# Optimization experiments

Hardware: AMD Instinct MI355X
Metric: run time of the kernel (lower is better)

Reference implementation:

```python
import jax, jax.numpy as jnp
import numpy as np

DIM = 1024
SEQ = 4096


def setup_inputs() -> dict:
    key = jax.random.key(0)
    ks = jax.random.split(key, 7)
    s = 1.0 / np.sqrt(DIM)
    return {
        "X": jax.random.normal(ks[0], (SEQ, DIM), dtype=jnp.float32),
        "Wq": jax.random.uniform(ks[1], (DIM, DIM), jnp.float32, -s, s),
        "bq": jax.random.uniform(ks[2], (DIM,), jnp.float32, -s, s),
        "Wk": jax.random.uniform(ks[3], (DIM, DIM), jnp.float32, -s, s),
        "bk": jax.random.uniform(ks[4], (DIM,), jnp.float32, -s, s),
        "Wv": jax.random.uniform(ks[5], (DIM, DIM), jnp.float32, -s, s),
        "bv": jax.random.uniform(ks[6], (DIM,), jnp.float32, -s, s),
    }


def reference(X, Wq, bq, Wk, bk, Wv, bv):
    # QKV projections (nn.Linear: x @ W.T + b); here W stored as [in, out]
    Q = X @ Wq + bq            # [S, D]
    K = X @ Wk + bk            # [S, D]
    V = X @ Wv + bv            # [S, D]
    scale = 1.0 / jnp.sqrt(jnp.asarray(X.shape[-1], X.dtype))
    scores = (Q @ K.T) * scale  # [S, S]
    attn = jax.nn.softmax(scores, axis=-1)
    return attn @ V            # [S, D]
```

## Files before the change

kernel.cpp:

```cpp
#include <hip/hip_runtime.h>

typedef unsigned short u16;
typedef unsigned int u32;
typedef __bf16 bf16x8 __attribute__((ext_vector_type(8)));
typedef float f32x4 __attribute__((ext_vector_type(4)));
typedef u16 u16x4 __attribute__((ext_vector_type(4)));

__device__ __forceinline__ u16 f32_to_bf16(float f) {
    u32 u = __builtin_bit_cast(u32, f);
    u32 r = (u + 0x7fffu + ((u >> 16) & 1u)) >> 16;
    return (u16)r;
}

__device__ __forceinline__ void async_cp16(const u16* g, u16* l) {
    __builtin_amdgcn_global_load_lds(
        (const __attribute__((address_space(1))) u32*)g,
        (__attribute__((address_space(3))) u32*)l, 16, 0, 0);
}

#define GEMM_PROLOG(Aptr, Bptr, LDA, LDB)                                     \
    __shared__ u16 lds[16384];                                                \
    const int tid  = threadIdx.x;                                             \
    const int wid  = tid >> 6;                                                \
    const int lane = tid & 63;                                                \
    const int s0 = wid * 2, s1 = s0 + 1;                                      \
    const int rr = lane >> 2;                                                 \
    const int cc = (lane & 3) * 8;                                            \
    const u16* gA0 = (Aptr) + (size_t)(bm + s0 * 16 + rr) * (LDA) + cc;       \
    const u16* gA1 = (Aptr) + (size_t)(bm + s1 * 16 + rr) * (LDA) + cc;       \
    const u16* gB0 = (Bptr) + (size_t)(bn + s0 * 16 + rr) * (LDB) + cc;       \
    const u16* gB1 = (Bptr) + (size_t)(bn + s1 * 16 + rr) * (LDB) + cc;       \
    u16* lA0  = &lds[s0 * 512];                                               \
    u16* lA1  = &lds[s1 * 512];                                               \
    u16* lA0h = lA0 + 4096;                                                   \
    u16* lA1h = lA1 + 4096;                                                   \
    u16* lB0  = &lds[8192 + s0 * 512];                                        \
    u16* lB1  = &lds[8192 + s1 * 512];                                        \
    u16* lB0h = lB0 + 4096;                                                   \
    u16* lB1h = lB1 + 4096;                                                   \
    const int wm = (wid >> 1) * 64;                                           \
    const int wn = (wid & 1) * 64;                                            \
    const int row16 = lane & 15;                                              \
    const int quad  = lane >> 4;                                              \
    f32x4 acc[4][4];                                                          \
    const f32x4 zero = {0.f, 0.f, 0.f, 0.f};                                  \
    _Pragma("unroll")                                                         \
    for (int i = 0; i < 4; i++)                                               \
        _Pragma("unroll")                                                     \
        for (int j = 0; j < 4; j++) acc[i][j] = zero;

#define GEMM_KLOOP(KLEN)                                                      \
    for (int kt = 0; kt < (KLEN); kt += 64) {                                 \
        __syncthreads();                                                      \
        async_cp16(gA0, lA0);                                                 \
        async_cp16(gA1, lA1);                                                 \
        async_cp16(gA0 + 32, lA0h);                                           \
        async_cp16(gA1 + 32, lA1h);                                           \
        async_cp16(gB0, lB0);                                                 \
        async_cp16(gB1, lB1);                                                 \
        async_cp16(gB0 + 32, lB0h);                                           \
        async_cp16(gB1 + 32, lB1h);                                           \
        gA0 += 64; gA1 += 64; gB0 += 64; gB1 += 64;                           \
        __syncthreads();                                                      \
        _Pragma("unroll")                                                     \
        for (int h = 0; h < 2; h++) {                                         \
            bf16x8 fa[4], fb[4];                                              \
            _Pragma("unroll")                                                 \
            for (int im = 0; im < 4; im++)                                    \
                fa[im] = *(const bf16x8*)&lds[h * 4096 + (wm + im * 16 + row16) * 32 + quad * 8]; \
            _Pragma("unroll")                                                 \
            for (int in = 0; in < 4; in++)                                    \
                fb[in] = *(const bf16x8*)&lds[8192 + h * 4096 + (wn + in * 16 + row16) * 32 + quad * 8]; \
            _Pragma("unroll")                                                 \
            for (int im = 0; im < 4; im++)                                    \
                _Pragma("unroll")                                             \
                for (int in = 0; in < 4; in++)                                \
                    acc[im][in] = __builtin_amdgcn_mfma_f32_16x16x32_bf16(    \
                        fa[im], fb[in], acc[im][in], 0, 0, 0);                \
        }                                                                     \
    }

#define SWIZZLE_2D()                                                          \
    const int L   = blockIdx.x;                                               \
    const int id2 = L & 255;                                                  \
    const int bm  = (((id2 & 7) * 4) + (id2 >> 6)) * 128;                     \
    const int bn  = (((id2 >> 3) & 7) + (L >> 8) * 8) * 128;

__global__ __launch_bounds__(256, 4)
void gemm_qkv(const u16* __restrict__ A, const u16* __restrict__ B,
              u16* __restrict__ C, u16* __restrict__ Vt,
              const float* __restrict__ bias,
              int K, int lda, int ldb, int ldc)
{
    SWIZZLE_2D()
    GEMM_PROLOG(A, B, lda, ldb)
    GEMM_KLOOP(K)
    if (bn < 2048) {
        #pragma unroll
        for (int im = 0; im < 4; im++) {
            #pragma unroll
            for (int in = 0; in < 4; in++) {
                const int n = bn + wn + in * 16 + row16;
                const float bv = bias[n];
                #pragma unroll
                for (int r = 0; r < 4; r++) {
                    const int m = bm + wm + im * 16 + quad * 4 + r;
                    C[(size_t)m * ldc + n] = f32_to_bf16(acc[im][in][r] + bv);
                }
            }
        }
    } else {
        #pragma unroll
        for (int im = 0; im < 4; im++) {
            #pragma unroll
            for (int in = 0; in < 4; in++) {
                const int n = bn + wn + in * 16 + row16;
                const float bv = bias[n];
                const int d = n - 2048;
                const int m = bm + wm + im * 16 + quad * 4;
                u16x4 pk;
                #pragma unroll
                for (int r = 0; r < 4; r++)
                    pk[r] = f32_to_bf16(acc[im][in][r] + bv);
                *(u16x4*)&Vt[(size_t)d * 4096 + m] = pk;
            }
        }
    }
}

__global__ __launch_bounds__(256, 4)
void gemm_score_exp(const u16* __restrict__ A, const u16* __restrict__ B,
                    u16* __restrict__ P, float* __restrict__ rowsum,
                    int K, int lda, int ldb, int ldc, float scale)
{
    SWIZZLE_2D()
    GEMM_PROLOG(A, B, lda, ldb)
    GEMM_KLOOP(K)
    #pragma unroll
    for (int im = 0; im < 4; im++) {
        #pragma unroll
        for (int r = 0; r < 4; r++) {
            const int m = bm + wm + im * 16 + quad * 4 + r;
            float rs = 0.f;
            #pragma unroll
            for (int in = 0; in < 4; in++) {
                const int n = bn + wn + in * 16 + row16;
                float e = __expf(acc[im][in][r] * scale);
                P[(size_t)m * ldc + n] = f32_to_bf16(e);
                rs += e;
            }
            rs += __shfl_xor(rs, 1);
            rs += __shfl_xor(rs, 2);
            rs += __shfl_xor(rs, 4);
            rs += __shfl_xor(rs, 8);
            if (row16 == 0) atomicAdd(&rowsum[m], rs);
        }
    }
}

__global__ __launch_bounds__(256, 4)
void gemm_pv_splitk(const u16* __restrict__ A, const u16* __restrict__ B,
                    float* __restrict__ C0, float* __restrict__ C1,
                    float* __restrict__ C2, float* __restrict__ C3,
                    int Kq, int lda, int ldb, int ldc)
{
    const int id2 = blockIdx.x;
    const int bm  = (((id2 & 7) * 4) + (id2 >> 6)) * 128;
    const int bn  = ((id2 >> 3) & 7) * 128;
    const int z   = blockIdx.y;
    float* C = (z == 0) ? C0 : (z == 1) ? C1 : (z == 2) ? C2 : C3;
    const int koff = z * Kq;
    GEMM_PROLOG(A + koff, B + koff, lda, ldb)
    GEMM_KLOOP(Kq)
    #pragma unroll
    for (int im = 0; im < 4; im++) {
        #pragma unroll
        for (int in = 0; in < 4; in++) {
            const int n = bn + wn + in * 16 + row16;
            #pragma unroll
            for (int r = 0; r < 4; r++) {
                const int m = bm + wm + im * 16 + quad * 4 + r;
                C[(size_t)m * ldc + n] = acc[im][in][r];
            }
        }
    }
}

__global__ __launch_bounds__(256)
void reduce4_scale(float4* __restrict__ out, const float4* __restrict__ p1,
                   const float4* __restrict__ p2, const float4* __restrict__ p3,
                   const float* __restrict__ rowsum)
{
    const int i = blockIdx.x * 256 + threadIdx.x;
    const float inv = 1.0f / rowsum[i >> 8];
    float4 a = out[i], b = p1[i], c = p2[i], d = p3[i];
    a.x = (a.x + b.x + c.x + d.x) * inv;
    a.y = (a.y + b.y + c.y + d.y) * inv;
    a.z = (a.z + b.z + c.z + d.z) * inv;
    a.w = (a.w + b.w + c.w + d.w) * inv;
    out[i] = a;
}

__global__ __launch_bounds__(256)
void convert_x(const float4* __restrict__ X, uint2* __restrict__ Xb)
{
    const int i = blockIdx.x * 256 + threadIdx.x;
    float4 v = X[i];
    uint2 o;
    o.x = (u32)f32_to_bf16(v.x) | ((u32)f32_to_bf16(v.y) << 16);
    o.y = (u32)f32_to_bf16(v.z) | ((u32)f32_to_bf16(v.w) << 16);
    Xb[i] = o;
}

__global__ __launch_bounds__(256)
void transpose_w3(const float* __restrict__ W0, const float* __restrict__ W1,
                  const float* __restrict__ W2, u16* __restrict__ Wt)
{
    __shared__ float t[32][33];
    const int z  = blockIdx.z;
    const float* W = (z == 0) ? W0 : (z == 1) ? W1 : W2;
    u16* dst = Wt + (size_t)z * 1024 * 1024;
    const int bk = blockIdx.x * 32;
    const int bn = blockIdx.y * 32;
    const int tx = threadIdx.x & 31;
    const int ty = threadIdx.x >> 5;
    #pragma unroll
    for (int i = 0; i < 32; i += 8)
        t[ty + i][tx] = W[(size_t)(bk + ty + i) * 1024 + bn + tx];
    __syncthreads();
    #pragma unroll
    for (int i = 0; i < 32; i += 8)
        dst[(size_t)(bn + ty + i) * 1024 + bk + tx] = f32_to_bf16(t[tx][ty + i]);
}

__global__ __launch_bounds__(256)
void prep(const float* __restrict__ bq, const float* __restrict__ bk,
          const float* __restrict__ bv, float* __restrict__ b3,
          float* __restrict__ rowsum)
{
    const int i = blockIdx.x * 256 + threadIdx.x;
    if (i < 3072)
        b3[i] = (i < 1024) ? bq[i] : (i < 2048) ? bk[i - 1024] : bv[i - 2048];
    else
        rowsum[i - 3072] = 0.f;
}

extern "C" void kernel_launch(void* const* d_in, const int* in_sizes, int n_in,
                              void* d_out, int out_size, void* d_ws, size_t ws_size,
                              hipStream_t stream)
{
    const float* X  = (const float*)d_in[0];
    const float* Wq = (const float*)d_in[1];
    const float* bq = (const float*)d_in[2];
    const float* Wk = (const float*)d_in[3];
    const float* bk = (const float*)d_in[4];
    const float* Wv = (const float*)d_in[5];
    const float* bv = (const float*)d_in[6];
    float* out = (float*)d_out;

    char* ws = (char*)d_ws;
    u16*   P      = (u16*)ws;
    u16*   Xb     = (u16*)ws;
    u16*   WqkvT  = (u16*)(ws + (8u << 20));
    float* rowsum = (float*)(ws + (32u << 20));
    float* bias3  = (float*)(ws + (32u << 20) + (64u << 10));
    u16*   QKV    = (u16*)(ws + (33u << 20));
    float* p1     = (float*)(ws + (33u << 20));
    float* p2     = (float*)(ws + (49u << 20));
    float* p3     = (float*)(ws + (65u << 20));
    u16*   Vt     = (u16*)(ws + (82u << 20));

    convert_x<<<4096, 256, 0, stream>>>((const float4*)X, (uint2*)Xb);
    transpose_w3<<<dim3(32, 32, 3), 256, 0, stream>>>(Wq, Wk, Wv, WqkvT);
    prep<<<28, 256, 0, stream>>>(bq, bk, bv, bias3, rowsum);

    gemm_qkv<<<768, 256, 0, stream>>>(Xb, WqkvT, QKV, Vt, bias3,
        1024, 1024, 1024, 3072);

    gemm_score_exp<<<1024, 256, 0, stream>>>(QKV, QKV + 1024, P, rowsum,
        1024, 3072, 3072, 4096, 0.03125f);

    gemm_pv_splitk<<<dim3(256, 4), 256, 0, stream>>>(P, Vt, out, p1, p2, p3,
        1024, 4096, 4096, 1024);

    reduce4_scale<<<4096, 256, 0, stream>>>((float4*)out, (const float4*)p1,
        (const float4*)p2, (const float4*)p3, rowsum);
}
```

Baseline: 215.3 us.

## Double-buffer GEMM K-loop with async prefetch and merge prep kernels into one launch

The shared GEMM K-loop changes from 64-wide steps with two barriers per step to 32-wide steps over two ping-pong LDS buffers. The next tile's async global-to-LDS copy is issued before computing on the current tile, so load latency overlaps MFMA work and only one barrier per iteration remains. Separately, the three preprocessing kernels (X conversion, weight transpose, bias/rowsum init) are merged into one launch dispatched by block index, saving two kernel launches. The change relies on the async copies of the previous iteration being complete at the barrier, and halving the K step doubles the number of loop iterations.

```diff
diff --git a/kernel.cpp b/kernel.cpp
--- a/kernel.cpp
+++ b/kernel.cpp
@@ -32,12 +32,8 @@
     const u16* gB1 = (Bptr) + (size_t)(bn + s1 * 16 + rr) * (LDB) + cc;       \
     u16* lA0  = &lds[s0 * 512];                                               \
     u16* lA1  = &lds[s1 * 512];                                               \
-    u16* lA0h = lA0 + 4096;                                                   \
-    u16* lA1h = lA1 + 4096;                                                   \
-    u16* lB0  = &lds[8192 + s0 * 512];                                        \
-    u16* lB1  = &lds[8192 + s1 * 512];                                        \
-    u16* lB0h = lB0 + 4096;                                                   \
-    u16* lB1h = lB1 + 4096;                                                   \
+    u16* lB0  = &lds[4096 + s0 * 512];                                        \
+    u16* lB1  = &lds[4096 + s1 * 512];                                        \
     const int wm = (wid >> 1) * 64;                                           \
     const int wn = (wid & 1) * 64;                                            \
     const int row16 = lane & 15;                                              \
@@ -50,27 +46,31 @@
         for (int j = 0; j < 4; j++) acc[i][j] = zero;
 
 #define GEMM_KLOOP(KLEN)                                                      \
-    for (int kt = 0; kt < (KLEN); kt += 64) {                                 \
-        __syncthreads();                                                      \
+    {                                                                         \
         async_cp16(gA0, lA0);                                                 \
         async_cp16(gA1, lA1);                                                 \
-        async_cp16(gA0 + 32, lA0h);                                           \
-        async_cp16(gA1 + 32, lA1h);                                           \
         async_cp16(gB0, lB0);                                                 \
         async_cp16(gB1, lB1);                                                 \
-        async_cp16(gB0 + 32, lB0h);                                           \
-        async_cp16(gB1 + 32, lB1h);                                           \
-        gA0 += 64; gA1 += 64; gB0 += 64; gB1 += 64;                           \
-        __syncthreads();                                                      \
-        _Pragma("unroll")                                                     \
-        for (int h = 0; h < 2; h++) {                                         \
+        gA0 += 32; gA1 += 32; gB0 += 32; gB1 += 32;                           \
+        const int NIT = (KLEN) >> 5;                                          \
+        for (int it = 0; it < NIT; ++it) {                                    \
+            const int cur = (it & 1) << 13;       \
+            const int nxt = 8192 - cur;                                       \
+            __syncthreads();       \
+            if (it + 1 < NIT) {                                               \
+                async_cp16(gA0, lA0 + nxt);                                   \
+                async_cp16(gA1, lA1 + nxt);                                   \
+                async_cp16(gB0, lB0 + nxt);                                   \
+                async_cp16(gB1, lB1 + nxt);                                   \
+                gA0 += 32; gA1 += 32; gB0 += 32; gB1 += 32;                   \
+            }                                                                 \
             bf16x8 fa[4], fb[4];                                              \
             _Pragma("unroll")                                                 \
             for (int im = 0; im < 4; im++)                                    \
-                fa[im] = *(const bf16x8*)&lds[h * 4096 + (wm + im * 16 + row16) * 32 + quad * 8]; \
+                fa[im] = *(const bf16x8*)&lds[cur + (wm + im * 16 + row16) * 32 + quad * 8]; \
             _Pragma("unroll")                                                 \
             for (int in = 0; in < 4; in++)                                    \
-                fb[in] = *(const bf16x8*)&lds[8192 + h * 4096 + (wn + in * 16 + row16) * 32 + quad * 8]; \
+                fb[in] = *(const bf16x8*)&lds[cur + 4096 + (wn + in * 16 + row16) * 32 + quad * 8]; \
             _Pragma("unroll")                                                 \
             for (int im = 0; im < 4; im++)                                    \
                 _Pragma("unroll")                                             \
@@ -202,47 +202,46 @@
 }
 
 __global__ __launch_bounds__(256)
-void convert_x(const float4* __restrict__ X, uint2* __restrict__ Xb)
-{
-    const int i = blockIdx.x * 256 + threadIdx.x;
-    float4 v = X[i];
-    uint2 o;
-    o.x = (u32)f32_to_bf16(v.x) | ((u32)f32_to_bf16(v.y) << 16);
-    o.y = (u32)f32_to_bf16(v.z) | ((u32)f32_to_bf16(v.w) << 16);
-    Xb[i] = o;
-}
-
-__global__ __launch_bounds__(256)
-void transpose_w3(const float* __restrict__ W0, const float* __restrict__ W1,
-                  const float* __restrict__ W2, u16* __restrict__ Wt)
+void prep_all(const float4* __restrict__ X, uint2* __restrict__ Xb,
+              const float* __restrict__ W0, const float* __restrict__ W1,
+              const float* __restrict__ W2, u16* __restrict__ Wt,
+              const float* __restrict__ bq, const float* __restrict__ bk,
+              const float* __restrict__ bv, float* __restrict__ b3,
+              float* __restrict__ rowsum)
 {
     __shared__ float t[32][33];
-    const int z  = blockIdx.z;
-    const float* W = (z == 0) ? W0 : (z == 1) ? W1 : W2;
-    u16* dst = Wt + (size_t)z * 1024 * 1024;
-    const int bk = blockIdx.x * 32;
-    const int bn = blockIdx.y * 32;
-    const int tx = threadIdx.x & 31;
-    const int ty = threadIdx.x >> 5;
-    #pragma unroll
-    for (int i = 0; i < 32; i += 8)
-        t[ty + i][tx] = W[(size_t)(bk + ty + i) * 1024 + bn + tx];
-    __syncthreads();
-    #pragma unroll
-    for (int i = 0; i < 32; i += 8)
-        dst[(size_t)(bn + ty + i) * 1024 + bk + tx] = f32_to_bf16(t[tx][ty + i]);
-}
-
-__global__ __launch_bounds__(256)
-void prep(const float* __restrict__ bq, const float* __restrict__ bk,
-          const float* __restrict__ bv, float* __restrict__ b3,
-          float* __restrict__ rowsum)
-{
-    const int i = blockIdx.x * 256 + threadIdx.x;
-    if (i < 3072)
-        b3[i] = (i < 1024) ? bq[i] : (i < 2048) ? bk[i - 1024] : bv[i - 2048];
-    else
-        rowsum[i - 3072] = 0.f;
+    const int b = blockIdx.x;
+    if (b < 4096) {
+        const int i = b * 256 + threadIdx.x;
+        float4 v = X[i];
+        uint2 o;
+        o.x = (u32)f32_to_bf16(v.x) | ((u32)f32_to_bf16(v.y) << 16);
+        o.y = (u32)f32_to_bf16(v.z) | ((u32)f32_to_bf16(v.w) << 16);
+        Xb[i] = o;
+    } else if (b < 7168) {
+        const int tt = b - 4096;
+        const int z  = tt >> 10;
+        const int r  = tt & 1023;
+        const float* W = (z == 0) ? W0 : (z == 1) ? W1 : W2;
+        u16* dst = Wt + (size_t)z * 1024 * 1024;
+        const int bk2 = (r & 31) * 32;
+        const int bn2 = (r >> 5) * 32;
+        const int tx = threadIdx.x & 31;
+        const int ty = threadIdx.x >> 5;
+        #pragma unroll
+        for (int i = 0; i < 32; i += 8)
+            t[ty + i][tx] = W[(size_t)(bk2 + ty + i) * 1024 + bn2 + tx];
+        __syncthreads();
+        #pragma unroll
+        for (int i = 0; i < 32; i += 8)
+            dst[(size_t)(bn2 + ty + i) * 1024 + bk2 + tx] = f32_to_bf16(t[tx][ty + i]);
+    } else {
+        const int i = (b - 7168) * 256 + threadIdx.x;
+        if (i < 3072)
+            b3[i] = (i < 1024) ? bq[i] : (i < 2048) ? bk[i - 1024] : bv[i - 2048];
+        else
+            rowsum[i - 3072] = 0.f;
+    }
 }
 
 extern "C" void kernel_launch(void* const* d_in, const int* in_sizes, int n_in,
@@ -270,9 +269,8 @@
     float* p3     = (float*)(ws + (65u << 20));
     u16*   Vt     = (u16*)(ws + (82u << 20));
 
-    convert_x<<<4096, 256, 0, stream>>>((const float4*)X, (uint2*)Xb);
-    transpose_w3<<<dim3(32, 32, 3), 256, 0, stream>>>(Wq, Wk, Wv, WqkvT);
-    prep<<<28, 256, 0, stream>>>(bq, bk, bv, bias3, rowsum);
+    prep_all<<<7196, 256, 0, stream>>>((const float4*)X, (uint2*)Xb,
+        Wq, Wk, Wv, WqkvT, bq, bk, bv, bias3, rowsum);
 
     gemm_qkv<<<768, 256, 0, stream>>>(Xb, WqkvT, QKV, Vt, bias3,
         1024, 1024, 1024, 3072);
```

Measured after the change: 218.2 us. No clear change (+1.4%).
